# Kernel optimization log

Measured on AMD Instinct MI355X. Metric: run time of the kernel, lower is better.

The kernel has to match this reference:

```python
import jax, jax.numpy as jnp
import numpy as np

B, C, P, K, H = 8, 128, 100000, 14, 8  # batch, channels, points, cavities, heads
RADIUS = 0.5


def setup_inputs() -> dict:
    key = jax.random.key(0)
    ks = jax.random.split(key, 11)
    C2 = 2 * C
    s = 0.05
    return {
        "x": jax.random.normal(ks[0], (B, C, P), jnp.float32),
        "points": jax.random.uniform(ks[1], (P, 3), jnp.float32),
        "cavities": jax.random.uniform(ks[2], (K, 3), jnp.float32),
        "w1": jax.random.normal(ks[3], (K, C2, C), jnp.float32) * s,
        "b1": jnp.zeros((K, C2), jnp.float32),
        "w2": jax.random.normal(ks[4], (K, C, C2), jnp.float32) * s,
        "b2": jnp.zeros((K, C), jnp.float32),
        "in_w": jax.random.normal(ks[5], (3 * C, C), jnp.float32) * s,
        "in_b": jnp.zeros((3 * C,), jnp.float32),
        "out_w": jax.random.normal(ks[6], (C, C), jnp.float32) * s,
        "out_b": jnp.zeros((C,), jnp.float32),
    }


def reference(x, points, cavities, w1, b1, w2, b2, in_w, in_b, out_w, out_b):
    dtype = x.dtype
    # ---- cavity pooling: mean of x over points within RADIUS of each cavity ----
    d_cp = jnp.linalg.norm(points[None, :, :] - cavities[:, None, :], axis=-1)  # [K,P]
    mask = (d_cp < RADIUS).astype(dtype)                                        # [K,P]
    counts = mask.sum(axis=1)                                                   # [K]
    sums = jnp.einsum('bcp,kp->bkc', x, mask)                                   # [B,K,C]
    feat = jnp.where(counts[None, :, None] > 0,
                     sums / jnp.maximum(counts, 1.0)[None, :, None],
                     jnp.zeros((), dtype))                                      # [B,K,C]
    # ---- per-cavity MLP: tanh(relu(f @ W1^T + b1) @ W2^T + b2) ----
    h = jax.nn.relu(jnp.einsum('bkc,kdc->bkd', feat, w1) + b1[None])            # [B,K,2C]
    proc = jnp.tanh(jnp.einsum('bkd,kcd->bkc', h, w2) + b2[None])               # [B,K,C]
    # ---- multi-head self-attention over the K=14 cavities (torch MHA semantics) ----
    qkv = jnp.einsum('bkc,ec->bke', proc, in_w) + in_b                          # [B,K,3C]
    q, k_, v = jnp.split(qkv, 3, axis=-1)
    Dh = C // H
    def heads(t):
        return t.reshape(B, K, H, Dh).transpose(0, 2, 1, 3)                     # [B,H,K,Dh]
    qh, kh, vh = heads(q), heads(k_), heads(v)
    scores = jnp.einsum('bhqd,bhkd->bhqk', qh, kh) / np.float32(np.sqrt(Dh))
    attn = jax.nn.softmax(scores, axis=-1)
    oh = jnp.einsum('bhqk,bhkd->bhqd', attn, vh)
    o = oh.transpose(0, 2, 1, 3).reshape(B, K, C)
    attended = jnp.einsum('bkc,oc->bko', o, out_w) + out_b                      # [B,K,C]
    # ---- nearest-cavity gather-add back to every point ----
    d_pk = jnp.linalg.norm(cavities[None, :, :] - points[:, None, :], axis=-1)  # [P,K]
    nearest = jnp.argmin(d_pk, axis=1)                                          # [P]
    att_t = attended.transpose(0, 2, 1)                                         # [B,C,K]
    return x + att_t[:, :, nearest]                                             # [B,C,P]
```

## Files before the change

kernel.cpp:

```cpp
#include <hip/hip_runtime.h>
#include <hip/hip_bf16.h>
#include <math.h>

#define B_ 8
#define C_ 128
#define P_ 100000
#define K_ 14
#define H_ 8
#define DH_ 16
#define C2_ (2*C_)
#define E3_ (3*C_)
#define R2 0.25f

typedef float f32x4_t __attribute__((ext_vector_type(4)));

__device__ __forceinline__ int bitsel(unsigned m, int k) {
#if __has_builtin(__builtin_amdgcn_sbfe)
    return __builtin_amdgcn_sbfe((int)m, (unsigned)k, 1u);
#else
    return ((int)(m << (31 - k))) >> 31;
#endif
}

__global__ void geom_kernel(const float* __restrict__ pts,
                            const float* __restrict__ cav,
                            unsigned short* __restrict__ mask,
                            unsigned char* __restrict__ nearest,
                            int* __restrict__ counts) {
    __shared__ float cx[K_], cy[K_], cz[K_];
    __shared__ int sm[K_];
    int tid = threadIdx.x;
    if (tid < K_) {
        cx[tid] = cav[tid*3+0];
        cy[tid] = cav[tid*3+1];
        cz[tid] = cav[tid*3+2];
        sm[tid] = 0;
    }
    __syncthreads();
    int p = blockIdx.x * blockDim.x + tid;
    bool valid = (p < P_);
    int pc = valid ? p : (P_ - 1);
    float px = pts[pc*3+0], py = pts[pc*3+1], pz = pts[pc*3+2];
    unsigned m = 0;
    float best = 1e30f;
    int bi = 0;
    #pragma unroll
    for (int k = 0; k < K_; ++k) {
        float dx = px - cx[k], dy = py - cy[k], dz = pz - cz[k];
        float d2 = dx*dx + dy*dy + dz*dz;
        if (d2 < R2) m |= (1u << k);
        if (d2 < best) { best = d2; bi = k; }
    }
    if (valid) {
        mask[p] = (unsigned short)m;
        nearest[p] = (unsigned char)bi;
    }
    int lane = tid & 63;
    #pragma unroll
    for (int k = 0; k < K_; ++k) {
        unsigned long long bal = __ballot(valid && ((m >> k) & 1u));
        if (lane == 0) atomicAdd(&sm[k], (int)__popcll(bal));
    }
    __syncthreads();
    if (tid < K_) atomicAdd(&counts[tid], sm[tid]);
}

__global__ __launch_bounds__(512) void pool_kernel(const float* __restrict__ x,
                                                   const unsigned short* __restrict__ mask,
                                                   float* __restrict__ sums) {
    int r0 = blockIdx.x * 4;
    int tid = threadIdx.x;
    const float4* xr0 = (const float4*)(x + (size_t)(r0+0) * P_);
    const float4* xr1 = (const float4*)(x + (size_t)(r0+1) * P_);
    const float4* xr2 = (const float4*)(x + (size_t)(r0+2) * P_);
    const float4* xr3 = (const float4*)(x + (size_t)(r0+3) * P_);
    const ushort4* mr = (const ushort4*)mask;
    float acc[4][K_];
    #pragma unroll
    for (int r = 0; r < 4; ++r)
        #pragma unroll
        for (int k = 0; k < K_; ++k) acc[r][k] = 0.f;
    for (int i = tid; i < P_/4; i += 512) {
        ushort4 mv = mr[i];
        unsigned ma = mv.x, mb = mv.y, mc = mv.z, md = mv.w;
        float4 xv0 = xr0[i], xv1 = xr1[i], xv2 = xr2[i], xv3 = xr3[i];
        #pragma unroll
        for (int k = 0; k < K_; ++k) {
            float m0 = __int_as_float(bitsel(ma, k) & 0x3f800000);
            float m1 = __int_as_float(bitsel(mb, k) & 0x3f800000);
            float m2 = __int_as_float(bitsel(mc, k) & 0x3f800000);
            float m3 = __int_as_float(bitsel(md, k) & 0x3f800000);
            acc[0][k] = fmaf(xv0.x, m0, fmaf(xv0.y, m1, fmaf(xv0.z, m2, fmaf(xv0.w, m3, acc[0][k]))));
            acc[1][k] = fmaf(xv1.x, m0, fmaf(xv1.y, m1, fmaf(xv1.z, m2, fmaf(xv1.w, m3, acc[1][k]))));
            acc[2][k] = fmaf(xv2.x, m0, fmaf(xv2.y, m1, fmaf(xv2.z, m2, fmaf(xv2.w, m3, acc[2][k]))));
            acc[3][k] = fmaf(xv3.x, m0, fmaf(xv3.y, m1, fmaf(xv3.z, m2, fmaf(xv3.w, m3, acc[3][k]))));
        }
    }
    int lane = tid & 63, wave = tid >> 6;
    __shared__ float lsum[8][4][K_];
    #pragma unroll
    for (int r = 0; r < 4; ++r) {
        #pragma unroll
        for (int k = 0; k < K_; ++k) {
            float v = acc[r][k];
            #pragma unroll
            for (int off = 32; off > 0; off >>= 1) v += __shfl_down(v, off);
            if (lane == 0) lsum[wave][r][k] = v;
        }
    }
    __syncthreads();
    if (tid < 4*K_) {
        int r = tid / K_, k = tid % K_;
        float t = 0.f;
        #pragma unroll
        for (int w = 0; w < 8; ++w) t += lsum[w][r][k];
        int row = r0 + r;
        int b = row >> 7, c = row & (C_-1);
        sums[((size_t)b*K_ + k)*C_ + c] = t;
    }
}

__global__ void mlp_kernel(const float* __restrict__ sums,
                           const int* __restrict__ counts,
                           const float* __restrict__ w1,
                           const float* __restrict__ b1,
                           const float* __restrict__ w2,
                           const float* __restrict__ b2,
                           const float* __restrict__ in_w,
                           const float* __restrict__ in_b,
                           float* __restrict__ qkv_out) {
    int b = blockIdx.x / K_, k = blockIdx.x % K_;
    int tid = threadIdx.x;
    __shared__ float feat[C_];
    __shared__ float h[C2_];
    __shared__ float pr[C_];
    int cnt = counts[k];
    float inv = (cnt > 0) ? (1.f / (float)cnt) : 0.f;
    if (tid < C_) feat[tid] = sums[((size_t)b*K_ + k)*C_ + tid] * inv;
    __syncthreads();
    {
        const float* w1r = w1 + ((size_t)k*C2_ + tid)*C_;
        float a = b1[k*C2_ + tid];
        #pragma unroll 8
        for (int c = 0; c < C_; ++c) a += feat[c] * w1r[c];
        h[tid] = fmaxf(a, 0.f);
    }
    __syncthreads();
    if (tid < C_) {
        const float* w2r = w2 + ((size_t)k*C_ + tid)*C2_;
        float a = b2[k*C_ + tid];
        #pragma unroll 8
        for (int d = 0; d < C2_; ++d) a += h[d] * w2r[d];
        pr[tid] = tanhf(a);
    }
    __syncthreads();
    for (int e = tid; e < E3_; e += 256) {
        const float* wr = in_w + (size_t)e*C_;
        float a = in_b[e];
        #pragma unroll 8
        for (int c = 0; c < C_; ++c) a += pr[c] * wr[c];
        qkv_out[((size_t)b*K_ + k)*E3_ + e] = a;
    }
}

__global__ void attn_kernel(const float* __restrict__ qkv_in,
                            const float* __restrict__ out_w,
                            const float* __restrict__ out_b,
                            float* __restrict__ att) {
    int b = blockIdx.x;
    int tid = threadIdx.x;
    __shared__ float qkv[K_][E3_];
    __shared__ float ov[K_][C_];
    for (int i = tid; i < K_*E3_; i += 256) qkv[i / E3_][i % E3_] = qkv_in[(size_t)b*K_*E3_ + i];
    __syncthreads();
    if (tid < H_*K_) {
        int hh = tid / K_, q = tid % K_;
        const float* qv = &qkv[q][hh*DH_];
        float sc[K_];
        float mx = -1e30f;
        #pragma unroll
        for (int kk = 0; kk < K_; ++kk) {
            float a = 0.f;
            #pragma unroll
            for (int d = 0; d < DH_; ++d) a += qv[d] * qkv[kk][C_ + hh*DH_ + d];
            a *= 0.25f;
            sc[kk] = a;
            mx = fmaxf(mx, a);
        }
        float ssum = 0.f;
        #pragma unroll
        for (int kk = 0; kk < K_; ++kk) { sc[kk] = __expf(sc[kk] - mx); ssum += sc[kk]; }
        float rinv = 1.f / ssum;
        #pragma unroll
        for (int d = 0; d < DH_; ++d) {
            float a = 0.f;
            #pragma unroll
            for (int kk = 0; kk < K_; ++kk) a += sc[kk] * qkv[kk][2*C_ + hh*DH_ + d];
            ov[q][hh*DH_ + d] = a * rinv;
        }
    }
    __syncthreads();
    for (int i = tid; i < K_*C_; i += 256) {
        int kk = i / C_, o = i % C_;
        const float* wr = out_w + (size_t)o*C_;
        float a = out_b[o];
        #pragma unroll 8
        for (int c = 0; c < C_; ++c) a += ov[kk][c] * wr[c];
        att[((size_t)b*K_ + kk)*C_ + o] = a;
    }
}

__global__ void gather_kernel(const float* __restrict__ x,
                              const float* __restrict__ att,
                              const unsigned char* __restrict__ nearest,
                              float* __restrict__ out) {
    int row = blockIdx.y;
    int b = row >> 7, c = row & (C_-1);
    __shared__ float al[K_];
    if (threadIdx.x < K_) al[threadIdx.x] = att[((size_t)b*K_ + threadIdx.x)*C_ + c];
    __syncthreads();
    const float4* xr = (const float4*)(x + (size_t)row * P_);
    f32x4_t* orow = (f32x4_t*)(out + (size_t)row * P_);
    const uchar4* nr = (const uchar4*)nearest;
    for (int j = blockIdx.x * blockDim.x + threadIdx.x; j < P_/4; j += 13*256) {
        int i = P_/4 - 1 - j;
        float4 xv = xr[i];
        uchar4 nv = nr[i];
        f32x4_t o;
        o.x = xv.x + al[nv.x];
        o.y = xv.y + al[nv.y];
        o.z = xv.z + al[nv.z];
        o.w = xv.w + al[nv.w];
        __builtin_nontemporal_store(o, &orow[i]);
    }
}

extern "C" void kernel_launch(void* const* d_in, const int* in_sizes, int n_in,
                              void* d_out, int out_size, void* d_ws, size_t ws_size,
                              hipStream_t stream) {
    const float* x      = (const float*)d_in[0];
    const float* points = (const float*)d_in[1];
    const float* cav    = (const float*)d_in[2];
    const float* w1     = (const float*)d_in[3];
    const float* b1     = (const float*)d_in[4];
    const float* w2     = (const float*)d_in[5];
    const float* b2     = (const float*)d_in[6];
    const float* in_w   = (const float*)d_in[7];
    const float* in_b   = (const float*)d_in[8];
    const float* out_w  = (const float*)d_in[9];
    const float* out_b  = (const float*)d_in[10];
    float* out = (float*)d_out;

    char* w = (char*)d_ws;
    unsigned short* mask    = (unsigned short*)(w + 0);
    unsigned char*  nearest = (unsigned char*)(w + 200192);
    int*            counts  = (int*)(w + 300288);
    float*          sums    = (float*)(w + 300544);
    float*          qkv     = (float*)(w + 358144);
    float*          att     = (float*)(w + 530432);

    (void)hipMemsetAsync(counts, 0, K_ * sizeof(int), stream);
    geom_kernel<<<(P_ + 255)/256, 256, 0, stream>>>(points, cav, mask, nearest, counts);
    pool_kernel<<<256, 512, 0, stream>>>(x, mask, sums);
    mlp_kernel<<<B_*K_, 256, 0, stream>>>(sums, counts, w1, b1, w2, b2, in_w, in_b, qkv);
    attn_kernel<<<B_, 256, 0, stream>>>(qkv, out_w, out_b, att);
    gather_kernel<<<dim3(13, B_*C_), 256, 0, stream>>>(x, att, nearest, out);
}
```

Measured before the change: 299.4 us.

## Pool with fp16 dot2 against pre-expanded per-cavity half mask planes

Adds an expand kernel that turns the 14-bit per-point mask into per-cavity planes of packed fp16 ones and zeros. The pooling kernel converts x to packed fp16 and accumulates with fdot2 instead of unpacking bits into fp32 FMAs, to cut ALU work in the masked sum. In exchange it reads 14 mask planes (about 2.8 MB) per iteration instead of one ushort4, and rounding x toward zero to fp16 loses precision. The gather kernel also switches from nontemporal stores to plain stores.

```diff
diff --git a/kernel.cpp b/kernel.cpp
--- a/kernel.cpp
+++ b/kernel.cpp
@@ -13,14 +13,7 @@
 #define R2 0.25f
 
 typedef float f32x4_t __attribute__((ext_vector_type(4)));
-
-__device__ __forceinline__ int bitsel(unsigned m, int k) {
-#if __has_builtin(__builtin_amdgcn_sbfe)
-    return __builtin_amdgcn_sbfe((int)m, (unsigned)k, 1u);
-#else
-    return ((int)(m << (31 - k))) >> 31;
-#endif
-}
+typedef __fp16 h2_t __attribute__((ext_vector_type(2)));
 
 __global__ void geom_kernel(const float* __restrict__ pts,
                             const float* __restrict__ cav,
@@ -65,8 +58,21 @@
     if (tid < K_) atomicAdd(&counts[tid], sm[tid]);
 }
 
+__global__ void expand_kernel(const unsigned short* __restrict__ mask,
+                              unsigned int* __restrict__ planes) {
+    int t = blockIdx.x * blockDim.x + threadIdx.x;
+    if (t >= P_/2) return;
+    unsigned m0 = mask[2*t], m1 = mask[2*t+1];
+    #pragma unroll
+    for (int k = 0; k < K_; ++k) {
+        unsigned lo = ((m0 >> k) & 1u) ? 0x3C00u : 0u;
+        unsigned hi = ((m1 >> k) & 1u) ? 0x3C000000u : 0u;
+        planes[(size_t)k*(P_/2) + t] = lo | hi;
+    }
+}
+
 __global__ __launch_bounds__(512) void pool_kernel(const float* __restrict__ x,
-                                                   const unsigned short* __restrict__ mask,
+                                                   const unsigned int* __restrict__ planes,
                                                    float* __restrict__ sums) {
     int r0 = blockIdx.x * 4;
     int tid = threadIdx.x;
@@ -74,26 +80,34 @@
     const float4* xr1 = (const float4*)(x + (size_t)(r0+1) * P_);
     const float4* xr2 = (const float4*)(x + (size_t)(r0+2) * P_);
     const float4* xr3 = (const float4*)(x + (size_t)(r0+3) * P_);
-    const ushort4* mr = (const ushort4*)mask;
     float acc[4][K_];
     #pragma unroll
     for (int r = 0; r < 4; ++r)
         #pragma unroll
         for (int k = 0; k < K_; ++k) acc[r][k] = 0.f;
     for (int i = tid; i < P_/4; i += 512) {
-        ushort4 mv = mr[i];
-        unsigned ma = mv.x, mb = mv.y, mc = mv.z, md = mv.w;
         float4 xv0 = xr0[i], xv1 = xr1[i], xv2 = xr2[i], xv3 = xr3[i];
+        h2_t a0 = __builtin_amdgcn_cvt_pkrtz(xv0.x, xv0.y);
+        h2_t b0 = __builtin_amdgcn_cvt_pkrtz(xv0.z, xv0.w);
+        h2_t a1 = __builtin_amdgcn_cvt_pkrtz(xv1.x, xv1.y);
+        h2_t b1 = __builtin_amdgcn_cvt_pkrtz(xv1.z, xv1.w);
+        h2_t a2 = __builtin_amdgcn_cvt_pkrtz(xv2.x, xv2.y);
+        h2_t b2 = __builtin_amdgcn_cvt_pkrtz(xv2.z, xv2.w);
+        h2_t a3 = __builtin_amdgcn_cvt_pkrtz(xv3.x, xv3.y);
+        h2_t b3 = __builtin_amdgcn_cvt_pkrtz(xv3.z, xv3.w);
         #pragma unroll
         for (int k = 0; k < K_; ++k) {
-            float m0 = __int_as_float(bitsel(ma, k) & 0x3f800000);
-            float m1 = __int_as_float(bitsel(mb, k) & 0x3f800000);
-            float m2 = __int_as_float(bitsel(mc, k) & 0x3f800000);
-            float m3 = __int_as_float(bitsel(md, k) & 0x3f800000);
-            acc[0][k] = fmaf(xv0.x, m0, fmaf(xv0.y, m1, fmaf(xv0.z, m2, fmaf(xv0.w, m3, acc[0][k]))));
-            acc[1][k] = fmaf(xv1.x, m0, fmaf(xv1.y, m1, fmaf(xv1.z, m2, fmaf(xv1.w, m3, acc[1][k]))));
-            acc[2][k] = fmaf(xv2.x, m0, fmaf(xv2.y, m1, fmaf(xv2.z, m2, fmaf(xv2.w, m3, acc[2][k]))));
-            acc[3][k] = fmaf(xv3.x, m0, fmaf(xv3.y, m1, fmaf(xv3.z, m2, fmaf(xv3.w, m3, acc[3][k]))));
+            uint2 mw = *(const uint2*)&planes[(size_t)k*(P_/2) + 2*i];
+            h2_t m01 = __builtin_bit_cast(h2_t, mw.x);
+            h2_t m23 = __builtin_bit_cast(h2_t, mw.y);
+            acc[0][k] = __builtin_amdgcn_fdot2(a0, m01, acc[0][k], false);
+            acc[0][k] = __builtin_amdgcn_fdot2(b0, m23, acc[0][k], false);
+            acc[1][k] = __builtin_amdgcn_fdot2(a1, m01, acc[1][k], false);
+            acc[1][k] = __builtin_amdgcn_fdot2(b1, m23, acc[1][k], false);
+            acc[2][k] = __builtin_amdgcn_fdot2(a2, m01, acc[2][k], false);
+            acc[2][k] = __builtin_amdgcn_fdot2(b2, m23, acc[2][k], false);
+            acc[3][k] = __builtin_amdgcn_fdot2(a3, m01, acc[3][k], false);
+            acc[3][k] = __builtin_amdgcn_fdot2(b3, m23, acc[3][k], false);
         }
     }
     int lane = tid & 63, wave = tid >> 6;
@@ -220,18 +234,18 @@
     if (threadIdx.x < K_) al[threadIdx.x] = att[((size_t)b*K_ + threadIdx.x)*C_ + c];
     __syncthreads();
     const float4* xr = (const float4*)(x + (size_t)row * P_);
-    f32x4_t* orow = (f32x4_t*)(out + (size_t)row * P_);
+    float4* orow = (float4*)(out + (size_t)row * P_);
     const uchar4* nr = (const uchar4*)nearest;
     for (int j = blockIdx.x * blockDim.x + threadIdx.x; j < P_/4; j += 13*256) {
         int i = P_/4 - 1 - j;
         float4 xv = xr[i];
         uchar4 nv = nr[i];
-        f32x4_t o;
+        float4 o;
         o.x = xv.x + al[nv.x];
         o.y = xv.y + al[nv.y];
         o.z = xv.z + al[nv.z];
         o.w = xv.w + al[nv.w];
-        __builtin_nontemporal_store(o, &orow[i]);
+        orow[i] = o;
     }
 }
 
@@ -258,10 +272,12 @@
     float*          sums    = (float*)(w + 300544);
     float*          qkv     = (float*)(w + 358144);
     float*          att     = (float*)(w + 530432);
+    unsigned int*   planes  = (unsigned int*)(w + 589824);
 
     (void)hipMemsetAsync(counts, 0, K_ * sizeof(int), stream);
     geom_kernel<<<(P_ + 255)/256, 256, 0, stream>>>(points, cav, mask, nearest, counts);
-    pool_kernel<<<256, 512, 0, stream>>>(x, mask, sums);
+    expand_kernel<<<(P_/2 + 255)/256, 256, 0, stream>>>(mask, planes);
+    pool_kernel<<<256, 512, 0, stream>>>(x, planes, sums);
     mlp_kernel<<<B_*K_, 256, 0, stream>>>(sums, counts, w1, b1, w2, b2, in_w, in_b, qkv);
     attn_kernel<<<B_, 256, 0, stream>>>(qkv, out_w, out_b, att);
     gather_kernel<<<dim3(13, B_*C_), 256, 0, stream>>>(x, att, nearest, out);
```

After: 372.0 us. 1.24x slower.

## Process batches in two halves so gather reuses x from cache

Applied to the files above, without the earlier changes.

Splits the pool/MLP/attention/gather pipeline into two passes over four batches each. Within each pass the pool kernel splits every row quad across two point segments, and the MLP sums the two partial results. The idea is that the gather for a half-batch reads x soon after pool read it, so x (about 205 MB per half) may stay partly in the large last-level cache. It also keeps the block count at 256 per pool launch. The cost is extra kernel launches and serialized small MLP and attention stages.

```diff
diff --git a/kernel.cpp b/kernel.cpp
--- a/kernel.cpp
+++ b/kernel.cpp
@@ -67,8 +67,11 @@
 
 __global__ __launch_bounds__(512) void pool_kernel(const float* __restrict__ x,
                                                    const unsigned short* __restrict__ mask,
-                                                   float* __restrict__ sums) {
-    int r0 = blockIdx.x * 4;
+                                                   float* __restrict__ partials,
+                                                   int row_base) {
+    int quad = blockIdx.x >> 1;
+    int seg  = blockIdx.x & 1;
+    int r0 = row_base + quad*4;
     int tid = threadIdx.x;
     const float4* xr0 = (const float4*)(x + (size_t)(r0+0) * P_);
     const float4* xr1 = (const float4*)(x + (size_t)(r0+1) * P_);
@@ -80,7 +83,9 @@
     for (int r = 0; r < 4; ++r)
         #pragma unroll
         for (int k = 0; k < K_; ++k) acc[r][k] = 0.f;
-    for (int i = tid; i < P_/4; i += 512) {
+    int i0 = seg * (P_/8);
+    int i1 = i0 + (P_/8);
+    for (int i = i0 + tid; i < i1; i += 512) {
         ushort4 mv = mr[i];
         unsigned ma = mv.x, mb = mv.y, mc = mv.z, md = mv.w;
         float4 xv0 = xr0[i], xv1 = xr1[i], xv2 = xr2[i], xv3 = xr3[i];
@@ -114,13 +119,13 @@
         float t = 0.f;
         #pragma unroll
         for (int w = 0; w < 8; ++w) t += lsum[w][r][k];
-        int row = r0 + r;
-        int b = row >> 7, c = row & (C_-1);
-        sums[((size_t)b*K_ + k)*C_ + c] = t;
-    }
-}
-
-__global__ void mlp_kernel(const float* __restrict__ sums,
+        int lrow = (r0 - row_base) + r;
+        int lb = lrow >> 7, c = lrow & (C_-1);
+        partials[(((size_t)seg*4 + lb)*K_ + k)*C_ + c] = t;
+    }
+}
+
+__global__ void mlp_kernel(const float* __restrict__ partials,
                            const int* __restrict__ counts,
                            const float* __restrict__ w1,
                            const float* __restrict__ b1,
@@ -128,15 +133,21 @@
                            const float* __restrict__ b2,
                            const float* __restrict__ in_w,
                            const float* __restrict__ in_b,
-                           float* __restrict__ qkv_out) {
-    int b = blockIdx.x / K_, k = blockIdx.x % K_;
+                           float* __restrict__ qkv_out,
+                           int b_base) {
+    int lb = blockIdx.x / K_, k = blockIdx.x % K_;
+    int b = b_base + lb;
     int tid = threadIdx.x;
     __shared__ float feat[C_];
     __shared__ float h[C2_];
     __shared__ float pr[C_];
     int cnt = counts[k];
     float inv = (cnt > 0) ? (1.f / (float)cnt) : 0.f;
-    if (tid < C_) feat[tid] = sums[((size_t)b*K_ + k)*C_ + tid] * inv;
+    if (tid < C_) {
+        float s = partials[(((size_t)0*4 + lb)*K_ + k)*C_ + tid]
+                + partials[(((size_t)1*4 + lb)*K_ + k)*C_ + tid];
+        feat[tid] = s * inv;
+    }
     __syncthreads();
     {
         const float* w1r = w1 + ((size_t)k*C2_ + tid)*C_;
@@ -166,8 +177,9 @@
 __global__ void attn_kernel(const float* __restrict__ qkv_in,
                             const float* __restrict__ out_w,
                             const float* __restrict__ out_b,
-                            float* __restrict__ att) {
-    int b = blockIdx.x;
+                            float* __restrict__ att,
+                            int b_base) {
+    int b = b_base + blockIdx.x;
     int tid = threadIdx.x;
     __shared__ float qkv[K_][E3_];
     __shared__ float ov[K_][C_];
@@ -213,8 +225,9 @@
 __global__ void gather_kernel(const float* __restrict__ x,
                               const float* __restrict__ att,
                               const unsigned char* __restrict__ nearest,
-                              float* __restrict__ out) {
-    int row = blockIdx.y;
+                              float* __restrict__ out,
+                              int row_base) {
+    int row = row_base + blockIdx.y;
     int b = row >> 7, c = row & (C_-1);
     __shared__ float al[K_];
     if (threadIdx.x < K_) al[threadIdx.x] = att[((size_t)b*K_ + threadIdx.x)*C_ + c];
@@ -255,14 +268,18 @@
     unsigned short* mask    = (unsigned short*)(w + 0);
     unsigned char*  nearest = (unsigned char*)(w + 200192);
     int*            counts  = (int*)(w + 300288);
-    float*          sums    = (float*)(w + 300544);
+    float*          partials= (float*)(w + 300544);
     float*          qkv     = (float*)(w + 358144);
     float*          att     = (float*)(w + 530432);
 
     (void)hipMemsetAsync(counts, 0, K_ * sizeof(int), stream);
     geom_kernel<<<(P_ + 255)/256, 256, 0, stream>>>(points, cav, mask, nearest, counts);
-    pool_kernel<<<256, 512, 0, stream>>>(x, mask, sums);
-    mlp_kernel<<<B_*K_, 256, 0, stream>>>(sums, counts, w1, b1, w2, b2, in_w, in_b, qkv);
-    attn_kernel<<<B_, 256, 0, stream>>>(qkv, out_w, out_b, att);
-    gather_kernel<<<dim3(13, B_*C_), 256, 0, stream>>>(x, att, nearest, out);
-}
+    for (int g = 0; g < 2; ++g) {
+        int row_base = g * 4 * C_;
+        int b_base   = g * 4;
+        pool_kernel<<<256, 512, 0, stream>>>(x, mask, partials, row_base);
+        mlp_kernel<<<4*K_, 256, 0, stream>>>(partials, counts, w1, b1, w2, b2, in_w, in_b, qkv, b_base);
+        attn_kernel<<<4, 256, 0, stream>>>(qkv, out_w, out_b, att, b_base);
+        gather_kernel<<<dim3(13, 4*C_), 256, 0, stream>>>(x, att, nearest, out, row_base);
+    }
+}
```

Result: slower. 359.2 us (+20.0%).

## Pool with bf16 MFMA matrix ops and process four rows per gather block

Applied to the files above, without the earlier changes.

Masked pooling is recast as a matrix multiply on 16x16x32 bf16 MFMA instructions. Each wave handles 32 channel rows against the 14-cavity mask bits, and per-split partial sums are written out and reduced inside the MLP kernel. This replaces scalar FMA work on the bit-unpacked mask. The gather kernel now handles four rows per block so the nearest-index loads are shared, and it uses ordinary stores instead of nontemporal ones. Rounding x to bf16 loses precision in the pooled means, which could push results past tolerance.

```diff
diff --git a/kernel.cpp b/kernel.cpp
--- a/kernel.cpp
+++ b/kernel.cpp
@@ -12,7 +12,8 @@
 #define E3_ (3*C_)
 #define R2 0.25f
 
-typedef float f32x4_t __attribute__((ext_vector_type(4)));
+typedef short bf16x8 __attribute__((ext_vector_type(8)));
+typedef float f32x4v __attribute__((ext_vector_type(4)));
 
 __device__ __forceinline__ int bitsel(unsigned m, int k) {
 #if __has_builtin(__builtin_amdgcn_sbfe)
@@ -20,6 +21,11 @@
 #else
     return ((int)(m << (31 - k))) >> 31;
 #endif
+}
+
+__device__ __forceinline__ short f2bfs(float f) {
+    __hip_bfloat16 h = __float2bfloat16(f);
+    return *reinterpret_cast<short*>(&h);
 }
 
 __global__ void geom_kernel(const float* __restrict__ pts,
@@ -65,62 +71,58 @@
     if (tid < K_) atomicAdd(&counts[tid], sm[tid]);
 }
 
-__global__ __launch_bounds__(512) void pool_kernel(const float* __restrict__ x,
-                                                   const unsigned short* __restrict__ mask,
-                                                   float* __restrict__ sums) {
-    int r0 = blockIdx.x * 4;
-    int tid = threadIdx.x;
-    const float4* xr0 = (const float4*)(x + (size_t)(r0+0) * P_);
-    const float4* xr1 = (const float4*)(x + (size_t)(r0+1) * P_);
-    const float4* xr2 = (const float4*)(x + (size_t)(r0+2) * P_);
-    const float4* xr3 = (const float4*)(x + (size_t)(r0+3) * P_);
-    const ushort4* mr = (const ushort4*)mask;
-    float acc[4][K_];
-    #pragma unroll
-    for (int r = 0; r < 4; ++r)
-        #pragma unroll
-        for (int k = 0; k < K_; ++k) acc[r][k] = 0.f;
-    for (int i = tid; i < P_/4; i += 512) {
-        ushort4 mv = mr[i];
-        unsigned ma = mv.x, mb = mv.y, mc = mv.z, md = mv.w;
-        float4 xv0 = xr0[i], xv1 = xr1[i], xv2 = xr2[i], xv3 = xr3[i];
-        #pragma unroll
-        for (int k = 0; k < K_; ++k) {
-            float m0 = __int_as_float(bitsel(ma, k) & 0x3f800000);
-            float m1 = __int_as_float(bitsel(mb, k) & 0x3f800000);
-            float m2 = __int_as_float(bitsel(mc, k) & 0x3f800000);
-            float m3 = __int_as_float(bitsel(md, k) & 0x3f800000);
-            acc[0][k] = fmaf(xv0.x, m0, fmaf(xv0.y, m1, fmaf(xv0.z, m2, fmaf(xv0.w, m3, acc[0][k]))));
-            acc[1][k] = fmaf(xv1.x, m0, fmaf(xv1.y, m1, fmaf(xv1.z, m2, fmaf(xv1.w, m3, acc[1][k]))));
-            acc[2][k] = fmaf(xv2.x, m0, fmaf(xv2.y, m1, fmaf(xv2.z, m2, fmaf(xv2.w, m3, acc[2][k]))));
-            acc[3][k] = fmaf(xv3.x, m0, fmaf(xv3.y, m1, fmaf(xv3.z, m2, fmaf(xv3.w, m3, acc[3][k]))));
-        }
-    }
-    int lane = tid & 63, wave = tid >> 6;
-    __shared__ float lsum[8][4][K_];
+__global__ __launch_bounds__(256) void pool_mfma_kernel(const float* __restrict__ x,
+                                                        const unsigned short* __restrict__ mask,
+                                                        float* __restrict__ partials) {
+    int gpair = blockIdx.x & 31;
+    int split = blockIdx.x >> 5;
+    int tid = threadIdx.x;
+    int wave = tid >> 6, lane = tid & 63;
+    int lrow = lane & 15, lgrp = lane >> 4;
+    int stripe = split*4 + wave;
+    const float* xr0 = x + (size_t)((2*gpair+0)*16 + lrow) * P_;
+    const float* xr1 = x + (size_t)((2*gpair+1)*16 + lrow) * P_;
+    f32x4v acc0 = {0.f,0.f,0.f,0.f}, acc1 = {0.f,0.f,0.f,0.f};
+    for (int t = stripe; t < P_/32; t += 32) {
+        int p0 = t*32 + lgrp*8;
+        ushort4 mw0 = *(const ushort4*)(mask + p0);
+        ushort4 mw1 = *(const ushort4*)(mask + p0 + 4);
+        float4 xa = *(const float4*)(xr0 + p0);
+        float4 xb = *(const float4*)(xr0 + p0 + 4);
+        float4 xc = *(const float4*)(xr1 + p0);
+        float4 xd = *(const float4*)(xr1 + p0 + 4);
+        bf16x8 bfr, a0, a1;
+        bfr[0] = (short)(bitsel(mw0.x, lrow) & 0x3F80);
+        bfr[1] = (short)(bitsel(mw0.y, lrow) & 0x3F80);
+        bfr[2] = (short)(bitsel(mw0.z, lrow) & 0x3F80);
+        bfr[3] = (short)(bitsel(mw0.w, lrow) & 0x3F80);
+        bfr[4] = (short)(bitsel(mw1.x, lrow) & 0x3F80);
+        bfr[5] = (short)(bitsel(mw1.y, lrow) & 0x3F80);
+        bfr[6] = (short)(bitsel(mw1.z, lrow) & 0x3F80);
+        bfr[7] = (short)(bitsel(mw1.w, lrow) & 0x3F80);
+        a0[0] = f2bfs(xa.x); a0[1] = f2bfs(xa.y); a0[2] = f2bfs(xa.z); a0[3] = f2bfs(xa.w);
+        a0[4] = f2bfs(xb.x); a0[5] = f2bfs(xb.y); a0[6] = f2bfs(xb.z); a0[7] = f2bfs(xb.w);
+        a1[0] = f2bfs(xc.x); a1[1] = f2bfs(xc.y); a1[2] = f2bfs(xc.z); a1[3] = f2bfs(xc.w);
+        a1[4] = f2bfs(xd.x); a1[5] = f2bfs(xd.y); a1[6] = f2bfs(xd.z); a1[7] = f2bfs(xd.w);
+        acc0 = __builtin_amdgcn_mfma_f32_16x16x32_bf16(a0, bfr, acc0, 0, 0, 0);
+        acc1 = __builtin_amdgcn_mfma_f32_16x16x32_bf16(a1, bfr, acc1, 0, 0, 0);
+    }
+    __shared__ float red[4][2][16][16];
     #pragma unroll
     for (int r = 0; r < 4; ++r) {
-        #pragma unroll
-        for (int k = 0; k < K_; ++k) {
-            float v = acc[r][k];
-            #pragma unroll
-            for (int off = 32; off > 0; off >>= 1) v += __shfl_down(v, off);
-            if (lane == 0) lsum[wave][r][k] = v;
-        }
-    }
-    __syncthreads();
-    if (tid < 4*K_) {
-        int r = tid / K_, k = tid % K_;
-        float t = 0.f;
-        #pragma unroll
-        for (int w = 0; w < 8; ++w) t += lsum[w][r][k];
-        int row = r0 + r;
-        int b = row >> 7, c = row & (C_-1);
-        sums[((size_t)b*K_ + k)*C_ + c] = t;
-    }
-}
-
-__global__ void mlp_kernel(const float* __restrict__ sums,
+        red[wave][0][lgrp*4 + r][lrow] = acc0[r];
+        red[wave][1][lgrp*4 + r][lrow] = acc1[r];
+    }
+    __syncthreads();
+    for (int i = tid; i < 512; i += 256) {
+        int cg = i >> 8, rr = (i >> 4) & 15, kk = i & 15;
+        float s = red[0][cg][rr][kk] + red[1][cg][rr][kk]
+                + red[2][cg][rr][kk] + red[3][cg][rr][kk];
+        partials[(((size_t)(2*gpair+cg))*8 + split)*256 + rr*16 + kk] = s;
+    }
+}
+
+__global__ void mlp_kernel(const float* __restrict__ partials,
                            const int* __restrict__ counts,
                            const float* __restrict__ w1,
                            const float* __restrict__ b1,
@@ -136,7 +138,14 @@
     __shared__ float pr[C_];
     int cnt = counts[k];
     float inv = (cnt > 0) ? (1.f / (float)cnt) : 0.f;
-    if (tid < C_) feat[tid] = sums[((size_t)b*K_ + k)*C_ + tid] * inv;
+    if (tid < C_) {
+        int cg = b*8 + (tid >> 4), rr = tid & 15;
+        const float* pp = partials + ((size_t)cg*8)*256 + rr*16 + k;
+        float s = 0.f;
+        #pragma unroll
+        for (int sp = 0; sp < 8; ++sp) s += pp[sp*256];
+        feat[tid] = s * inv;
+    }
     __syncthreads();
     {
         const float* w1r = w1 + ((size_t)k*C2_ + tid)*C_;
@@ -214,24 +223,33 @@
                               const float* __restrict__ att,
                               const unsigned char* __restrict__ nearest,
                               float* __restrict__ out) {
-    int row = blockIdx.y;
-    int b = row >> 7, c = row & (C_-1);
-    __shared__ float al[K_];
-    if (threadIdx.x < K_) al[threadIdx.x] = att[((size_t)b*K_ + threadIdx.x)*C_ + c];
-    __syncthreads();
-    const float4* xr = (const float4*)(x + (size_t)row * P_);
-    f32x4_t* orow = (f32x4_t*)(out + (size_t)row * P_);
+    int r0 = blockIdx.y * 4;
+    int b = r0 >> 7;
+    __shared__ float al[4][K_];
+    if (threadIdx.x < 4*K_) {
+        int r = threadIdx.x / K_, kk = threadIdx.x % K_;
+        al[r][kk] = att[((size_t)b*K_ + kk)*C_ + ((r0 + r) & (C_-1))];
+    }
+    __syncthreads();
+    const float4* xr0 = (const float4*)(x + (size_t)(r0+0) * P_);
+    const float4* xr1 = (const float4*)(x + (size_t)(r0+1) * P_);
+    const float4* xr2 = (const float4*)(x + (size_t)(r0+2) * P_);
+    const float4* xr3 = (const float4*)(x + (size_t)(r0+3) * P_);
+    float4* o0 = (float4*)(out + (size_t)(r0+0) * P_);
+    float4* o1 = (float4*)(out + (size_t)(r0+1) * P_);
+    float4* o2 = (float4*)(out + (size_t)(r0+2) * P_);
+    float4* o3 = (float4*)(out + (size_t)(r0+3) * P_);
     const uchar4* nr = (const uchar4*)nearest;
     for (int j = blockIdx.x * blockDim.x + threadIdx.x; j < P_/4; j += 13*256) {
         int i = P_/4 - 1 - j;
-        float4 xv = xr[i];
         uchar4 nv = nr[i];
-        f32x4_t o;
-        o.x = xv.x + al[nv.x];
-        o.y = xv.y + al[nv.y];
-        o.z = xv.z + al[nv.z];
-        o.w = xv.w + al[nv.w];
-        __builtin_nontemporal_store(o, &orow[i]);
+        float4 x0 = xr0[i], x1 = xr1[i], x2 = xr2[i], x3 = xr3[i];
+        float4 v0, v1, v2, v3;
+        v0.x = x0.x + al[0][nv.x]; v0.y = x0.y + al[0][nv.y]; v0.z = x0.z + al[0][nv.z]; v0.w = x0.w + al[0][nv.w];
+        v1.x = x1.x + al[1][nv.x]; v1.y = x1.y + al[1][nv.y]; v1.z = x1.z + al[1][nv.z]; v1.w = x1.w + al[1][nv.w];
+        v2.x = x2.x + al[2][nv.x]; v2.y = x2.y + al[2][nv.y]; v2.z = x2.z + al[2][nv.z]; v2.w = x2.w + al[2][nv.w];
+        v3.x = x3.x + al[3][nv.x]; v3.y = x3.y + al[3][nv.y]; v3.z = x3.z + al[3][nv.z]; v3.w = x3.w + al[3][nv.w];
+        o0[i] = v0; o1[i] = v1; o2[i] = v2; o3[i] = v3;
     }
 }
 
@@ -255,14 +273,14 @@
     unsigned short* mask    = (unsigned short*)(w + 0);
     unsigned char*  nearest = (unsigned char*)(w + 200192);
     int*            counts  = (int*)(w + 300288);
-    float*          sums    = (float*)(w + 300544);
-    float*          qkv     = (float*)(w + 358144);
-    float*          att     = (float*)(w + 530432);
+    float*          partials= (float*)(w + 300544);
+    float*          qkv     = (float*)(w + 824832);
+    float*          att     = (float*)(w + 996864);
 
     (void)hipMemsetAsync(counts, 0, K_ * sizeof(int), stream);
     geom_kernel<<<(P_ + 255)/256, 256, 0, stream>>>(points, cav, mask, nearest, counts);
-    pool_kernel<<<256, 512, 0, stream>>>(x, mask, sums);
-    mlp_kernel<<<B_*K_, 256, 0, stream>>>(sums, counts, w1, b1, w2, b2, in_w, in_b, qkv);
+    pool_mfma_kernel<<<256, 256, 0, stream>>>(x, mask, partials);
+    mlp_kernel<<<B_*K_, 256, 0, stream>>>(partials, counts, w1, b1, w2, b2, in_w, in_b, qkv);
     attn_kernel<<<B_, 256, 0, stream>>>(qkv, out_w, out_b, att);
-    gather_kernel<<<dim3(13, B_*C_), 256, 0, stream>>>(x, att, nearest, out);
-}
+    gather_kernel<<<dim3(13, 256), 256, 0, stream>>>(x, att, nearest, out);
+}
```

Result: slower. 323.7 us (+8.1%).
